# Performance work log

Measured on AMD Instinct MI355X. Metric: run time of the kernel, lower is better.

Reference implementation:

```python
import jax, jax.numpy as jnp
import numpy as np

HEAD_SIZE = 128  # embeddings_dims // no_of_heads = 4096 // 32


def apply_rope(v):
    # v: [B, S, d] with d = HEAD_SIZE; interleaved-pair rotation as in source
    B, S, d = v.shape
    pos = jnp.arange(S, dtype=jnp.float32)[:, None]              # [S, 1]
    idx = jnp.arange(0, d, 2, dtype=jnp.float32)[None, :]        # [1, d//2]
    theta = jnp.power(10000.0, -2.0 * idx / d)                   # [1, d//2]
    angles = pos * theta                                         # [S, d//2]
    cos = jnp.cos(angles)
    sin = jnp.sin(angles)
    vr = v.reshape(B, S, d // 2, 2)
    x0, x1 = vr[..., 0], vr[..., 1]
    out = jnp.stack([x0 * cos - x1 * sin, x1 * cos + x0 * sin], axis=-1)
    return out.reshape(B, S, d)


def setup_inputs() -> dict:
    key = jax.random.key(0)
    kx, kq, kk, kv = jax.random.split(key, 4)
    B, S, D = 2, 4096, 4096
    d = HEAD_SIZE
    scale = 1.0 / np.sqrt(D)
    return {
        "x": jax.random.normal(kx, (B, S, D), dtype=jnp.float32),
        "Wq": jax.random.normal(kq, (d, D), dtype=jnp.float32) * scale,
        "Wk": jax.random.normal(kk, (d, D), dtype=jnp.float32) * scale,
        "Wv": jax.random.normal(kv, (d, D), dtype=jnp.float32) * scale,
    }


def reference(x, Wq, Wk, Wv):
    # single attention head, non-flash path (eval mode: dropout = identity)
    B, S, D = x.shape
    q = jnp.einsum('bsd,hd->bsh', x, Wq)  # [B, S, head]
    k = jnp.einsum('bsd,hd->bsh', x, Wk)
    v = jnp.einsum('bsd,hd->bsh', x, Wv)
    q = apply_rope(q)
    k = apply_rope(k)
    scale = k.shape[-1] ** (-0.5)
    scores = jnp.einsum('bqh,bkh->bqk', q, k) * scale  # [B, S, S]
    causal = jnp.tril(jnp.ones((S, S), dtype=bool))
    scores = jnp.where(causal, scores, -jnp.inf)
    weights = jax.nn.softmax(scores, axis=-1)
    out = jnp.einsum('bqk,bkh->bqh', weights, v)  # [B, S, head]
    return out
```

## Files before the change

kernel.cpp:

```cpp
#include <hip/hip_runtime.h>

typedef _Float16 half8 __attribute__((ext_vector_type(8)));
typedef _Float16 half2v __attribute__((ext_vector_type(2)));
typedef float f32x4 __attribute__((ext_vector_type(4)));

#define S_LEN 4096
#define D_DIM 4096
#define HD 128


__device__ __forceinline__ void gload_lds16(const _Float16* g, _Float16* l) {
    __builtin_amdgcn_global_load_lds(
        (const __attribute__((address_space(1))) unsigned int*)g,
        (__attribute__((address_space(3))) unsigned int*)l, 16, 0, 0);
}

__global__ __launch_bounds__(256) void convw_kernel(const float* __restrict__ wq,
                                                    const float* __restrict__ wk,
                                                    const float* __restrict__ wv,
                                                    _Float16* __restrict__ wh) {
    const int g = blockIdx.x * 256 + threadIdx.x;
    const int p = g >> 16;
    const int off = (g & 65535) * 8;
    const float* src = ((p == 0) ? wq : (p == 1) ? wk : wv) + off;
    float4 v0 = *(const float4*)src;
    float4 v1 = *(const float4*)(src + 4);
    half8 h = { (_Float16)v0.x, (_Float16)v0.y, (_Float16)v0.z, (_Float16)v0.w,
                (_Float16)v1.x, (_Float16)v1.y, (_Float16)v1.z, (_Float16)v1.w };
    *(half8*)&wh[(size_t)p * 524288 + off] = h;
}

#define QSTR 136
template<int KSPLIT>
__global__ __launch_bounds__(256) void proj_kernel(const float* __restrict__ x,
                                                   const _Float16* __restrict__ wh,
                                                   _Float16* __restrict__ qw,
                                                   _Float16* __restrict__ kw,
                                                   _Float16* __restrict__ vt,
                                                   float* __restrict__ P) {
    __shared__ __align__(16) _Float16 smem[17408];
    const int tid = threadIdx.x;
    const int wg = blockIdx.x;
    const int nwg = 384 * KSPLIT;
    const int swz = (wg & 7) * (nwg >> 3) + (wg >> 3);
    const int bx = swz % 3;
    const int rest = swz / 3;
    const int ks = (KSPLIT == 2) ? (rest & 1) : 0;
    const int M0 = ((KSPLIT == 2) ? (rest >> 1) : rest) * 64;
    const int NS = 128 / KSPLIT;
    const int lane = tid & 63, wv_ = tid >> 6;
    const int l15 = lane & 15, quad = lane >> 4;

    const int arow = tid >> 2, acol = (tid & 3) * 8;
    const float* xa = x + (size_t)(M0 + arow) * D_DIM + acol + ks * (D_DIM / 2);
    const _Float16* wsrc = wh + (size_t)bx * 128 * D_DIM + ks * (D_DIM / 2) +
                           (size_t)(wv_ * 32 + l15) * D_DIM + quad * 8;

    const int awoff = ((arow >> 4) * 64 + (arow & 15) + (tid & 3) * 16) * 8;
    const int rdoff = lane * 8;

    f32x4 acc[4][2];
    for (int mi = 0; mi < 4; ++mi)
        for (int ni = 0; ni < 2; ++ni)
            acc[mi][ni] = (f32x4){0.f, 0.f, 0.f, 0.f};

    auto stageA = [&](_Float16* buf, float4 A0, float4 A1) {
        half8 ha = { (_Float16)A0.x, (_Float16)A0.y, (_Float16)A0.z, (_Float16)A0.w,
                     (_Float16)A1.x, (_Float16)A1.y, (_Float16)A1.z, (_Float16)A1.w };
        *(half8*)&buf[awoff] = ha;
    };
    auto stageB = [&](_Float16* buf, int slab) {
        const _Float16* s = wsrc + slab * 32;
        gload_lds16(s,               &buf[2048 + wv_ * 1024]);
        gload_lds16(s + 16 * D_DIM,  &buf[2048 + wv_ * 1024 + 512]);
    };
    auto compute = [&](const _Float16* buf) {
        const _Float16* Af = buf + rdoff;
        const _Float16* Bf = buf + 2048 + wv_ * 1024 + rdoff;
        half8 af[4], bf[2];
        for (int mi = 0; mi < 4; ++mi)
            af[mi] = *(const half8*)(Af + mi * 512);
        for (int ni = 0; ni < 2; ++ni)
            bf[ni] = *(const half8*)(Bf + ni * 512);
        for (int mi = 0; mi < 4; ++mi)
            for (int ni = 0; ni < 2; ++ni)
                acc[mi][ni] = __builtin_amdgcn_mfma_f32_16x16x32_f16(af[mi], bf[ni],
                                                                     acc[mi][ni], 0, 0, 0);
    };

    float4 a0_0, a0_1, a1_0, a1_1;
    a0_0 = *(const float4*)(xa);      a0_1 = *(const float4*)(xa + 4);
    a1_0 = *(const float4*)(xa + 32); a1_1 = *(const float4*)(xa + 36);
    stageB(smem, 0);

    for (int i = 0; i < NS; i += 2) {
        stageA(smem, a0_0, a0_1);
        __syncthreads();
        if (i + 2 < NS) {
            a0_0 = *(const float4*)(xa + (i + 2) * 32);
            a0_1 = *(const float4*)(xa + (i + 2) * 32 + 4);
        }
        stageB(smem + 6144, i + 1);
        compute(smem);
        stageA(smem + 6144, a1_0, a1_1);
        __syncthreads();
        if (i + 3 < NS) {
            a1_0 = *(const float4*)(xa + (i + 3) * 32);
            a1_1 = *(const float4*)(xa + (i + 3) * 32 + 4);
        }
        if (i + 2 < NS) stageB(smem, i + 2);
        compute(smem + 6144);
    }
    __syncthreads();

    if (KSPLIT == 2) {
        float* sf = (float*)smem;
        for (int mi = 0; mi < 4; ++mi)
            for (int ni = 0; ni < 2; ++ni)
                for (int r = 0; r < 4; ++r)
                    sf[(mi * 16 + quad * 4 + r) * 132 + wv_ * 32 + ni * 16 + l15] =
                        acc[mi][ni][r];
        __syncthreads();
        const int row = tid >> 2, c0 = (tid & 3) * 32;
        float* dst = P + ((size_t)(ks * 3 + bx) * 8192 + M0 + row) * HD + c0;
        for (int j = 0; j < 8; ++j)
            *(float4*)(dst + j * 4) = *(const float4*)&sf[row * 132 + c0 + j * 4];
    } else if (bx < 2) {
        for (int mi = 0; mi < 4; ++mi)
            for (int ni = 0; ni < 2; ++ni)
                for (int r = 0; r < 4; ++r)
                    smem[(mi * 16 + quad * 4 + r) * QSTR + wv_ * 32 + ni * 16 + l15] =
                        (_Float16)acc[mi][ni][r];
        __syncthreads();
        _Float16* dst = ((bx == 0) ? qw : kw) + (size_t)M0 * HD;
        const int row = tid >> 2, c0 = (tid & 3) * 32;
        for (int j = 0; j < 4; ++j)
            *(half8*)&dst[row * HD + c0 + j * 8] = *(const half8*)&smem[row * QSTR + c0 + j * 8];
    } else {
        for (int mi = 0; mi < 4; ++mi)
            for (int ni = 0; ni < 2; ++ni)
                for (int r = 0; r < 4; ++r)
                    smem[(wv_ * 32 + ni * 16 + l15) * QSTR + mi * 16 + quad * 4 + r] =
                        (_Float16)acc[mi][ni][r];
        __syncthreads();
        _Float16* dst = vt + (size_t)(M0 >> 12) * HD * S_LEN + (M0 & (S_LEN - 1));
        const int hd = tid >> 1, s0 = (tid & 1) * 32;
        for (int j = 0; j < 4; ++j)
            *(half8*)&dst[(size_t)hd * S_LEN + s0 + j * 8] =
                *(const half8*)&smem[hd * QSTR + s0 + j * 8];
    }
}

__global__ __launch_bounds__(256) void combine_kernel(const float* __restrict__ P,
                                                      _Float16* __restrict__ qw,
                                                      _Float16* __restrict__ kw,
                                                      _Float16* __restrict__ vt) {
    const int tid = threadIdx.x;
    const int M0 = blockIdx.x * 64;
    const int row = tid >> 2, c0 = (tid & 3) * 32;
    if (blockIdx.y == 0) {
        const float* Pq0 = P + ((size_t)0 * 8192 + M0 + row) * HD + c0;
        const float* Pq1 = P + ((size_t)3 * 8192 + M0 + row) * HD + c0;
        const float* Pk0 = P + ((size_t)1 * 8192 + M0 + row) * HD + c0;
        const float* Pk1 = P + ((size_t)4 * 8192 + M0 + row) * HD + c0;
        float qv[32], kv[32];
#pragma unroll
        for (int j = 0; j < 8; ++j) {
            float4 a = *(const float4*)(Pq0 + j * 4);
            float4 b = *(const float4*)(Pq1 + j * 4);
            float4 c = *(const float4*)(Pk0 + j * 4);
            float4 d = *(const float4*)(Pk1 + j * 4);
            qv[j * 4 + 0] = a.x + b.x; qv[j * 4 + 1] = a.y + b.y;
            qv[j * 4 + 2] = a.z + b.z; qv[j * 4 + 3] = a.w + b.w;
            kv[j * 4 + 0] = c.x + d.x; kv[j * 4 + 1] = c.y + d.y;
            kv[j * 4 + 2] = c.z + d.z; kv[j * 4 + 3] = c.w + d.w;
        }
        const int s = (M0 + row) & (S_LEN - 1);
        half8 oq[4], ok[4];
#pragma unroll
        for (int jp = 0; jp < 16; ++jp) {
            const int pi = (c0 >> 1) + jp;
            const float theta = exp2f((float)pi * -0.4152410118609203f);
            float sn, cn;
            sincosf((float)s * theta, &sn, &cn);
            const float q0 = qv[2 * jp], q1 = qv[2 * jp + 1];
            const float k0 = kv[2 * jp], k1 = kv[2 * jp + 1];
            oq[jp >> 2][(2 * jp) & 7]     = (_Float16)(q0 * cn - q1 * sn);
            oq[jp >> 2][(2 * jp + 1) & 7] = (_Float16)(q1 * cn + q0 * sn);
            ok[jp >> 2][(2 * jp) & 7]     = (_Float16)(k0 * cn - k1 * sn);
            ok[jp >> 2][(2 * jp + 1) & 7] = (_Float16)(k1 * cn + k0 * sn);
        }
        _Float16* qdst = qw + (size_t)(M0 + row) * HD + c0;
        _Float16* kdst = kw + (size_t)(M0 + row) * HD + c0;
#pragma unroll
        for (int j = 0; j < 4; ++j) {
            *(half8*)(qdst + j * 8) = oq[j];
            *(half8*)(kdst + j * 8) = ok[j];
        }
    } else {
        __shared__ __align__(16) _Float16 sh[128][72];
        const float* Pv0 = P + ((size_t)2 * 8192 + M0 + row) * HD + c0;
        const float* Pv1 = P + ((size_t)5 * 8192 + M0 + row) * HD + c0;
#pragma unroll
        for (int j = 0; j < 8; ++j) {
            float4 a = *(const float4*)(Pv0 + j * 4);
            float4 b = *(const float4*)(Pv1 + j * 4);
            sh[c0 + j * 4 + 0][row] = (_Float16)(a.x + b.x);
            sh[c0 + j * 4 + 1][row] = (_Float16)(a.y + b.y);
            sh[c0 + j * 4 + 2][row] = (_Float16)(a.z + b.z);
            sh[c0 + j * 4 + 3][row] = (_Float16)(a.w + b.w);
        }
        __syncthreads();
        const int hd = tid >> 1, s0 = (tid & 1) * 32;
        _Float16* dst = vt + (size_t)(M0 >> 12) * HD * S_LEN + (size_t)hd * S_LEN +
                        (M0 & (S_LEN - 1)) + s0;
        for (int j = 0; j < 4; ++j)
            *(half8*)(dst + j * 8) = *(const half8*)&sh[hd][s0 + j * 8];
    }
}

__global__ __launch_bounds__(256) void rope_kernel(_Float16* __restrict__ qw,
                                                   _Float16* __restrict__ kw) {
    const int g = blockIdx.x * 256 + threadIdx.x;
    const int m = g >> 6, p = g & 63;
    const int s = m & (S_LEN - 1);
    const float theta = exp2f((float)p * -0.4152410118609203f);
    float sn, cn;
    sincosf((float)s * theta, &sn, &cn);
    const size_t off = (size_t)m * HD + 2 * p;
    half2v qv = *(half2v*)&qw[off];
    half2v kv = *(half2v*)&kw[off];
    float q0 = qv[0], q1 = qv[1], k0 = kv[0], k1 = kv[1];
    half2v qo = { (_Float16)(q0 * cn - q1 * sn), (_Float16)(q1 * cn + q0 * sn) };
    half2v ko = { (_Float16)(k0 * cn - k1 * sn), (_Float16)(k1 * cn + k0 * sn) };
    *(half2v*)&qw[off] = qo;
    *(half2v*)&kw[off] = ko;
}

__device__ __forceinline__ void load_kf(const _Float16* __restrict__ kb, int kbase,
                                        int l15, int quad, half8* kf) {
    const _Float16* kr = kb + (size_t)(kbase + l15) * HD + quad * 8;
    for (int kk = 0; kk < 4; ++kk) {
        kf[kk]     = *(const half8*)(kr + kk * 32);
        kf[4 + kk] = *(const half8*)(kr + 16 * HD + kk * 32);
    }
}

template<bool MASKED>
__device__ __forceinline__ void attn_tile(int kbase, int qg, int l15, int quad,
                                          const half8* kf,
                                          const _Float16* __restrict__ vtb,
                                          const half8* bq, f32x4* acc,
                                          float& mrun, float& lrun) {
    const float csc = 0.1275174348796053f;
    half8 va[8];
    const _Float16* vr = vtb + (size_t)l15 * S_LEN + kbase + quad * 8;
    for (int c = 0; c < 8; ++c)
        va[c] = *(const half8*)(vr + (size_t)c * 16 * S_LEN);
    f32x4 st0 = (f32x4){0.f, 0.f, 0.f, 0.f};
    f32x4 st1 = (f32x4){0.f, 0.f, 0.f, 0.f};
    for (int kk = 0; kk < 4; ++kk) {
        st0 = __builtin_amdgcn_mfma_f32_16x16x32_f16(kf[kk],     bq[kk], st0, 0, 0, 0);
        st1 = __builtin_amdgcn_mfma_f32_16x16x32_f16(kf[4 + kk], bq[kk], st1, 0, 0, 0);
    }
    float p0[4], p1[4];
    float mloc = -1e30f;
    for (int r = 0; r < 4; ++r) {
        float v0 = st0[r] * csc;
        float v1 = st1[r] * csc;
        if (MASKED) {
            const int key0 = kbase + quad * 4 + r;
            if (key0 > qg)      v0 = -1e30f;
            if (key0 + 16 > qg) v1 = -1e30f;
        }
        p0[r] = v0; p1[r] = v1;
        mloc = fmaxf(mloc, fmaxf(v0, v1));
    }
    mloc = fmaxf(mloc, __shfl_xor(mloc, 16));
    mloc = fmaxf(mloc, __shfl_xor(mloc, 32));
    const float mnew = fmaxf(mrun, mloc);
    const float alpha = exp2f(mrun - mnew);
    mrun = mnew;
    float ls = 0.f;
    for (int r = 0; r < 4; ++r) {
        p0[r] = exp2f(p0[r] - mnew);
        p1[r] = exp2f(p1[r] - mnew);
        ls += p0[r] + p1[r];
    }
    ls += __shfl_xor(ls, 16);
    ls += __shfl_xor(ls, 32);
    lrun = lrun * alpha + ls;
    for (int c = 0; c < 8; ++c)
        acc[c] *= alpha;
    int ph0 = __builtin_bit_cast(int, __builtin_amdgcn_cvt_pkrtz(p0[0], p0[1]));
    int ph1 = __builtin_bit_cast(int, __builtin_amdgcn_cvt_pkrtz(p0[2], p0[3]));
    int ph2 = __builtin_bit_cast(int, __builtin_amdgcn_cvt_pkrtz(p1[0], p1[1]));
    int ph3 = __builtin_bit_cast(int, __builtin_amdgcn_cvt_pkrtz(p1[2], p1[3]));
    const int s0 = (l15 + (((quad << 1)    ) & 3) * 16) * 4;
    const int s1 = (l15 + (((quad << 1) + 1) & 3) * 16) * 4;
    int a0 = __builtin_amdgcn_ds_bpermute(s0, ph0);
    int a1 = __builtin_amdgcn_ds_bpermute(s0, ph1);
    int a2 = __builtin_amdgcn_ds_bpermute(s1, ph0);
    int a3 = __builtin_amdgcn_ds_bpermute(s1, ph1);
    int b0 = __builtin_amdgcn_ds_bpermute(s0, ph2);
    int b1 = __builtin_amdgcn_ds_bpermute(s0, ph3);
    int b2 = __builtin_amdgcn_ds_bpermute(s1, ph2);
    int b3 = __builtin_amdgcn_ds_bpermute(s1, ph3);
    const bool lo = quad < 2;
    int4 pi = { lo ? a0 : b0, lo ? a1 : b1, lo ? a2 : b2, lo ? a3 : b3 };
    half8 pf = __builtin_bit_cast(half8, pi);
    for (int c = 0; c < 8; ++c)
        acc[c] = __builtin_amdgcn_mfma_f32_16x16x32_f16(va[c], pf, acc[c], 0, 0, 0);
}

__global__ __launch_bounds__(256) void attn_kernel(const _Float16* __restrict__ q,
                                                   const _Float16* __restrict__ k,
                                                   const _Float16* __restrict__ vt,
                                                   float* __restrict__ out) {
    __shared__ __align__(16) float Osh[4][16][132];
    __shared__ float msh[4][16];
    __shared__ float lsh[4][16];
    const int tid = threadIdx.x;
    const int lane = tid & 63, wv_ = tid >> 6;
    const int l15 = lane & 15, quad = lane >> 4;
    const int bidx = blockIdx.x;
    const int b = bidx & 1;
    const int t = 255 - (bidx >> 1);
    const int qb = t * 16;
    const int qg = qb + l15;

    const _Float16* qp = q + (size_t)(b * S_LEN + qb) * HD;
    half8 bq[4];
    for (int kk = 0; kk < 4; ++kk)
        bq[kk] = *(const half8*)&qp[l15 * HD + kk * 32 + quad * 8];

    f32x4 acc[8];
    for (int c = 0; c < 8; ++c) acc[c] = (f32x4){0.f, 0.f, 0.f, 0.f};
    float mrun = -1e30f, lrun = 0.f;

    const _Float16* kb = k + (size_t)b * S_LEN * HD;
    const _Float16* vtb = vt + (size_t)b * HD * S_LEN;

    const int nfull = (qb + 1) >> 5;
    const int kend = nfull * 32;
    const bool hasm = ((nfull & 3) == wv_);
    const int kb0 = wv_ * 32;

    half8 kf[8], kf2[8];
    if (kb0 < kend)      load_kf(kb, kb0, l15, quad, kf);
    else if (hasm)       load_kf(kb, kend, l15, quad, kf);
    for (int kbase = kb0; kbase < kend; kbase += 128) {
        const int kn = kbase + 128;
        if (kn < kend)   load_kf(kb, kn, l15, quad, kf2);
        else if (hasm)   load_kf(kb, kend, l15, quad, kf2);
        attn_tile<false>(kbase, qg, l15, quad, kf, vtb, bq, acc, mrun, lrun);
        for (int j = 0; j < 8; ++j) kf[j] = kf2[j];
    }
    if (hasm)
        attn_tile<true>(kend, qg, l15, quad, kf, vtb, bq, acc, mrun, lrun);

    for (int c = 0; c < 8; ++c)
        *(f32x4*)&Osh[wv_][l15][c * 16 + quad * 4] = acc[c];
    if (quad == 0) { msh[wv_][l15] = mrun; lsh[wv_][l15] = lrun; }
    __syncthreads();

    const int qr = tid >> 4, dg = (tid & 15) * 8;
    float m0 = msh[0][qr], m1 = msh[1][qr], m2 = msh[2][qr], m3 = msh[3][qr];
    float mm = fmaxf(fmaxf(m0, m1), fmaxf(m2, m3));
    float f0 = exp2f(m0 - mm), f1 = exp2f(m1 - mm), f2 = exp2f(m2 - mm), f3 = exp2f(m3 - mm);
    float l = lsh[0][qr] * f0 + lsh[1][qr] * f1 + lsh[2][qr] * f2 + lsh[3][qr] * f3;
    f32x4 oa = (f32x4){0.f, 0.f, 0.f, 0.f}, ob = oa;
    oa += *(f32x4*)&Osh[0][qr][dg] * f0;  ob += *(f32x4*)&Osh[0][qr][dg + 4] * f0;
    oa += *(f32x4*)&Osh[1][qr][dg] * f1;  ob += *(f32x4*)&Osh[1][qr][dg + 4] * f1;
    oa += *(f32x4*)&Osh[2][qr][dg] * f2;  ob += *(f32x4*)&Osh[2][qr][dg + 4] * f2;
    oa += *(f32x4*)&Osh[3][qr][dg] * f3;  ob += *(f32x4*)&Osh[3][qr][dg + 4] * f3;
    const float inv = 1.0f / l;
    float* op = out + (size_t)(b * S_LEN + qb + qr) * HD + dg;
    *(float4*)op       = (float4){oa[0] * inv, oa[1] * inv, oa[2] * inv, oa[3] * inv};
    *(float4*)(op + 4) = (float4){ob[0] * inv, ob[1] * inv, ob[2] * inv, ob[3] * inv};
}

extern "C" void kernel_launch(void* const* d_in, const int* in_sizes, int n_in,
                              void* d_out, int out_size, void* d_ws, size_t ws_size,
                              hipStream_t stream) {
    const float* x  = (const float*)d_in[0];
    const float* Wq = (const float*)d_in[1];
    const float* Wk = (const float*)d_in[2];
    const float* Wv = (const float*)d_in[3];
    float* out = (float*)d_out;
    char* ws = (char*)d_ws;
    _Float16* qw = (_Float16*)(ws);
    _Float16* kw = (_Float16*)(ws + (2u << 20));
    _Float16* vt = (_Float16*)(ws + (4u << 20));
    _Float16* wh = (_Float16*)(ws + (6u << 20));
    float* P = (float*)(ws + (9u << 20));

    const size_t need2 = (size_t)(9u << 20) + (size_t)2 * 3 * 8192 * 128 * 4;
    convw_kernel<<<dim3(768), dim3(256), 0, stream>>>(Wq, Wk, Wv, wh);
    if (ws_size >= need2) {
        proj_kernel<2><<<dim3(768), dim3(256), 0, stream>>>(x, wh, qw, kw, vt, P);
        combine_kernel<<<dim3(128, 2), dim3(256), 0, stream>>>(P, qw, kw, vt);
    } else {
        proj_kernel<1><<<dim3(384), dim3(256), 0, stream>>>(x, wh, qw, kw, vt, P);
        rope_kernel<<<dim3(2048), dim3(256), 0, stream>>>(qw, kw);
    }
    attn_kernel<<<dim3(512), dim3(256), 0, stream>>>(qw, kw, vt, out);
}
```

Baseline: 343.4 us.

## Precompute RoPE table, double-buffer K/V loads, skip unneeded softmax rescale

Adds a small kernel that precomputes a cos/sin table, so combine_kernel reads it instead of calling sincosf per element. The attention loop now prefetches V alongside K and unrolls by two with ping-pong register buffers. The online-softmax rescale of acc and lrun is skipped when no lane's max increased, and attn_kernel gets a launch-bounds occupancy hint of 2. The aim is to hide V load latency and cut transcendental and ALU work, at the cost of higher register pressure and an extra kernel launch.

```diff
diff --git a/kernel.cpp b/kernel.cpp
--- a/kernel.cpp
+++ b/kernel.cpp
@@ -28,6 +28,15 @@
     half8 h = { (_Float16)v0.x, (_Float16)v0.y, (_Float16)v0.z, (_Float16)v0.w,
                 (_Float16)v1.x, (_Float16)v1.y, (_Float16)v1.z, (_Float16)v1.w };
     *(half8*)&wh[(size_t)p * 524288 + off] = h;
+}
+
+__global__ __launch_bounds__(256) void trig_kernel(float* __restrict__ tab) {
+    const int g = blockIdx.x * 256 + threadIdx.x;
+    const int s = g >> 6, p = g & 63;
+    const float theta = exp2f((float)p * -0.4152410118609203f);
+    float sn, cn;
+    sincosf((float)s * theta, &sn, &cn);
+    *(float2*)&tab[g * 2] = (float2){cn, sn};
 }
 
 #define QSTR 136
@@ -55,7 +64,6 @@
     const float* xa = x + (size_t)(M0 + arow) * D_DIM + acol + ks * (D_DIM / 2);
     const _Float16* wsrc = wh + (size_t)bx * 128 * D_DIM + ks * (D_DIM / 2) +
                            (size_t)(wv_ * 32 + l15) * D_DIM + quad * 8;
-
     const int awoff = ((arow >> 4) * 64 + (arow & 15) + (tid & 3) * 16) * 8;
     const int rdoff = lane * 8;
 
@@ -71,8 +79,8 @@
     };
     auto stageB = [&](_Float16* buf, int slab) {
         const _Float16* s = wsrc + slab * 32;
-        gload_lds16(s,               &buf[2048 + wv_ * 1024]);
-        gload_lds16(s + 16 * D_DIM,  &buf[2048 + wv_ * 1024 + 512]);
+        gload_lds16(s,              &buf[2048 + wv_ * 1024]);
+        gload_lds16(s + 16 * D_DIM, &buf[2048 + wv_ * 1024 + 512]);
     };
     auto compute = [&](const _Float16* buf) {
         const _Float16* Af = buf + rdoff;
@@ -152,6 +160,7 @@
 }
 
 __global__ __launch_bounds__(256) void combine_kernel(const float* __restrict__ P,
+                                                      const float* __restrict__ tab,
                                                       _Float16* __restrict__ qw,
                                                       _Float16* __restrict__ kw,
                                                       _Float16* __restrict__ vt) {
@@ -176,13 +185,12 @@
             kv[j * 4 + 2] = c.z + d.z; kv[j * 4 + 3] = c.w + d.w;
         }
         const int s = (M0 + row) & (S_LEN - 1);
+        const float2* tb = (const float2*)tab + s * 64 + (c0 >> 1);
         half8 oq[4], ok[4];
 #pragma unroll
         for (int jp = 0; jp < 16; ++jp) {
-            const int pi = (c0 >> 1) + jp;
-            const float theta = exp2f((float)pi * -0.4152410118609203f);
-            float sn, cn;
-            sincosf((float)s * theta, &sn, &cn);
+            const float2 cs = tb[jp];
+            const float cn = cs.x, sn = cs.y;
             const float q0 = qv[2 * jp], q1 = qv[2 * jp + 1];
             const float k0 = kv[2 * jp], k1 = kv[2 * jp + 1];
             oq[jp >> 2][(2 * jp) & 7]     = (_Float16)(q0 * cn - q1 * sn);
@@ -246,17 +254,19 @@
     }
 }
 
+__device__ __forceinline__ void load_vf(const _Float16* __restrict__ vtb, int kbase,
+                                        int l15, int quad, half8* va) {
+    const _Float16* vr = vtb + (size_t)l15 * S_LEN + kbase + quad * 8;
+    for (int c = 0; c < 8; ++c)
+        va[c] = *(const half8*)(vr + (size_t)c * 16 * S_LEN);
+}
+
 template<bool MASKED>
 __device__ __forceinline__ void attn_tile(int kbase, int qg, int l15, int quad,
-                                          const half8* kf,
-                                          const _Float16* __restrict__ vtb,
+                                          const half8* kf, const half8* va,
                                           const half8* bq, f32x4* acc,
                                           float& mrun, float& lrun) {
     const float csc = 0.1275174348796053f;
-    half8 va[8];
-    const _Float16* vr = vtb + (size_t)l15 * S_LEN + kbase + quad * 8;
-    for (int c = 0; c < 8; ++c)
-        va[c] = *(const half8*)(vr + (size_t)c * 16 * S_LEN);
     f32x4 st0 = (f32x4){0.f, 0.f, 0.f, 0.f};
     f32x4 st1 = (f32x4){0.f, 0.f, 0.f, 0.f};
     for (int kk = 0; kk < 4; ++kk) {
@@ -278,20 +288,23 @@
     }
     mloc = fmaxf(mloc, __shfl_xor(mloc, 16));
     mloc = fmaxf(mloc, __shfl_xor(mloc, 32));
-    const float mnew = fmaxf(mrun, mloc);
-    const float alpha = exp2f(mrun - mnew);
-    mrun = mnew;
+    if (__any(mloc > mrun)) {
+        const float mnew = fmaxf(mrun, mloc);
+        const float alpha = exp2f(mrun - mnew);
+        lrun *= alpha;
+        for (int c = 0; c < 8; ++c)
+            acc[c] *= alpha;
+        mrun = mnew;
+    }
     float ls = 0.f;
     for (int r = 0; r < 4; ++r) {
-        p0[r] = exp2f(p0[r] - mnew);
-        p1[r] = exp2f(p1[r] - mnew);
+        p0[r] = exp2f(p0[r] - mrun);
+        p1[r] = exp2f(p1[r] - mrun);
         ls += p0[r] + p1[r];
     }
     ls += __shfl_xor(ls, 16);
     ls += __shfl_xor(ls, 32);
-    lrun = lrun * alpha + ls;
-    for (int c = 0; c < 8; ++c)
-        acc[c] *= alpha;
+    lrun += ls;
     int ph0 = __builtin_bit_cast(int, __builtin_amdgcn_cvt_pkrtz(p0[0], p0[1]));
     int ph1 = __builtin_bit_cast(int, __builtin_amdgcn_cvt_pkrtz(p0[2], p0[3]));
     int ph2 = __builtin_bit_cast(int, __builtin_amdgcn_cvt_pkrtz(p1[0], p1[1]));
@@ -313,10 +326,10 @@
         acc[c] = __builtin_amdgcn_mfma_f32_16x16x32_f16(va[c], pf, acc[c], 0, 0, 0);
 }
 
-__global__ __launch_bounds__(256) void attn_kernel(const _Float16* __restrict__ q,
-                                                   const _Float16* __restrict__ k,
-                                                   const _Float16* __restrict__ vt,
-                                                   float* __restrict__ out) {
+__global__ __launch_bounds__(256, 2) void attn_kernel(const _Float16* __restrict__ q,
+                                                      const _Float16* __restrict__ k,
+                                                      const _Float16* __restrict__ vt,
+                                                      float* __restrict__ out) {
     __shared__ __align__(16) float Osh[4][16][132];
     __shared__ float msh[4][16];
     __shared__ float lsh[4][16];
@@ -346,18 +359,26 @@
     const bool hasm = ((nfull & 3) == wv_);
     const int kb0 = wv_ * 32;
 
-    half8 kf[8], kf2[8];
-    if (kb0 < kend)      load_kf(kb, kb0, l15, quad, kf);
-    else if (hasm)       load_kf(kb, kend, l15, quad, kf);
-    for (int kbase = kb0; kbase < kend; kbase += 128) {
+    half8 kA[8], vA[8], kB[8], vB[8];
+    if (kb0 < kend) { load_kf(kb, kb0, l15, quad, kA);  load_vf(vtb, kb0, l15, quad, vA); }
+    else if (hasm)  { load_kf(kb, kend, l15, quad, kA); load_vf(vtb, kend, l15, quad, vA); }
+    for (int kbase = kb0; kbase < kend; kbase += 256) {
         const int kn = kbase + 128;
-        if (kn < kend)   load_kf(kb, kn, l15, quad, kf2);
-        else if (hasm)   load_kf(kb, kend, l15, quad, kf2);
-        attn_tile<false>(kbase, qg, l15, quad, kf, vtb, bq, acc, mrun, lrun);
-        for (int j = 0; j < 8; ++j) kf[j] = kf2[j];
-    }
-    if (hasm)
-        attn_tile<true>(kend, qg, l15, quad, kf, vtb, bq, acc, mrun, lrun);
+        if (kn < kend)  { load_kf(kb, kn, l15, quad, kB);   load_vf(vtb, kn, l15, quad, vB); }
+        else if (hasm)  { load_kf(kb, kend, l15, quad, kB); load_vf(vtb, kend, l15, quad, vB); }
+        attn_tile<false>(kbase, qg, l15, quad, kA, vA, bq, acc, mrun, lrun);
+        if (kn < kend) {
+            const int kn2 = kbase + 256;
+            if (kn2 < kend) { load_kf(kb, kn2, l15, quad, kA);  load_vf(vtb, kn2, l15, quad, vA); }
+            else if (hasm)  { load_kf(kb, kend, l15, quad, kA); load_vf(vtb, kend, l15, quad, vA); }
+            attn_tile<false>(kn, qg, l15, quad, kB, vB, bq, acc, mrun, lrun);
+        }
+    }
+    if (hasm) {
+        const int nf = (kb0 < kend) ? ((kend - kb0 + 127) >> 7) : 0;
+        if (nf & 1) attn_tile<true>(kend, qg, l15, quad, kB, vB, bq, acc, mrun, lrun);
+        else        attn_tile<true>(kend, qg, l15, quad, kA, vA, bq, acc, mrun, lrun);
+    }
 
     for (int c = 0; c < 8; ++c)
         *(f32x4*)&Osh[wv_][l15][c * 16 + quad * 4] = acc[c];
@@ -393,13 +414,15 @@
     _Float16* kw = (_Float16*)(ws + (2u << 20));
     _Float16* vt = (_Float16*)(ws + (4u << 20));
     _Float16* wh = (_Float16*)(ws + (6u << 20));
-    float* P = (float*)(ws + (9u << 20));
-
-    const size_t need2 = (size_t)(9u << 20) + (size_t)2 * 3 * 8192 * 128 * 4;
+    float* P   = (float*)(ws + (9u << 20));
+    float* tab = (float*)(ws + (33u << 20));
+
+    const size_t need = (size_t)(35u << 20);
     convw_kernel<<<dim3(768), dim3(256), 0, stream>>>(Wq, Wk, Wv, wh);
-    if (ws_size >= need2) {
+    if (ws_size >= need) {
+        trig_kernel<<<dim3(1024), dim3(256), 0, stream>>>(tab);
         proj_kernel<2><<<dim3(768), dim3(256), 0, stream>>>(x, wh, qw, kw, vt, P);
-        combine_kernel<<<dim3(128, 2), dim3(256), 0, stream>>>(P, qw, kw, vt);
+        combine_kernel<<<dim3(128, 2), dim3(256), 0, stream>>>(P, tab, qw, kw, vt);
     } else {
         proj_kernel<1><<<dim3(384), dim3(256), 0, stream>>>(x, wh, qw, kw, vt, P);
         rope_kernel<<<dim3(2048), dim3(256), 0, stream>>>(qw, kw);
```

New measurement: 346.0 us. About the same (+0.8%).
